# Performance work log

Measured on AMD Instinct MI355X. Metric: run time of the kernel, lower is better.

## Reference

```python
import jax, jax.numpy as jnp
import numpy as np

B, T, FEAT, H, E, NT, NH = 64, 256, 188, 512, 1024, 14, 8
HD = E // NH  # head dim = 128


def _gru_dir(x, w_ih, w_hh, b_ih, b_hh):
    # x: [T, B, in]; PyTorch GRU gate order: r, z, n
    xp = jnp.einsum('tbi,gi->tbg', x, w_ih) + b_ih  # [T,B,3H]

    def step(h, xt):
        hp = h @ w_hh.T + b_hh
        r = jax.nn.sigmoid(xt[..., :H] + hp[..., :H])
        z = jax.nn.sigmoid(xt[..., H:2 * H] + hp[..., H:2 * H])
        n = jnp.tanh(xt[..., 2 * H:] + r * hp[..., 2 * H:])
        h = (1 - z) * n + z * h
        return h, h

    h0 = jnp.zeros((x.shape[1], H), x.dtype)
    _, hs = jax.lax.scan(step, h0, xp)
    return hs  # [T,B,H]


def _bigru(x, wf, wb):
    f = _gru_dir(x, *wf)
    b = _gru_dir(x[::-1], *wb)[::-1]
    return jnp.concatenate([f, b], -1)  # [T,B,2H]


def _forward(features, ne_table, g1f, g1b, g2f, g2b, q_w, q_b, k_w, k_b, v_w, v_b,
             out_w, out_b, lin_w, lin_b, crf_start, crf_end, crf_trans, labels):
    nb = features.shape[0]
    x = features.transpose(1, 0, 2)  # [T,B,FEAT]
    enc = _bigru(x, g1f, g1b)        # [T,B,2H]=[T,B,E]
    # NE embedding: arange(14) rows for every batch element -> [S=14, B, 14]
    ne = jnp.broadcast_to(ne_table[:, None, :], (NT, nb, NT))
    # nn.MultiheadAttention with kdim=vdim=NT
    q = (enc @ q_w.T + q_b).reshape(T, nb, NH, HD)
    k = (ne @ k_w.T + k_b).reshape(NT, nb, NH, HD)
    v = (ne @ v_w.T + v_b).reshape(NT, nb, NH, HD)
    scores = jnp.einsum('tbhd,sbhd->bhts', q, k) / jnp.sqrt(jnp.float32(HD))
    attn = jax.nn.softmax(scores, axis=-1)
    ao = jnp.einsum('bhts,sbhd->tbhd', attn, v).reshape(T, nb, E)
    ao = ao @ out_w.T + out_b
    dec_in = jnp.concatenate([enc, ao], -1)   # [T,B,4H]
    dec = _bigru(dec_in, g2f, g2b)            # [T,B,2H]
    dec = dec @ lin_w.T + lin_b               # [T,B,NT]
    dec = dec.transpose(1, 0, 2)              # [B,T,NT]
    # scaled dot product against NE embeddings -> emissions [B,T,NT]
    logits = jnp.einsum('btd,sd->bts', dec, ne_table) / jnp.sqrt(jnp.float32(NT))
    # CRF negative log likelihood, reduction='mean', full mask
    em = jnp.take_along_axis(logits, labels[..., None], axis=2)[..., 0]  # [B,T]
    num = (crf_start[labels[:, 0]] + em.sum(1)
           + crf_trans[labels[:, :-1], labels[:, 1:]].sum(1)
           + crf_end[labels[:, -1]])
    alpha0 = crf_start + logits[:, 0]  # [B,NT]

    def step(a, e_t):
        a = jax.nn.logsumexp(a[:, :, None] + crf_trans[None] + e_t[:, None, :], axis=1)
        return a, None

    alpha, _ = jax.lax.scan(step, alpha0, logits[:, 1:].transpose(1, 0, 2))
    den = jax.nn.logsumexp(alpha + crf_end, axis=1)
    return -(num - den).mean()


def setup_inputs() -> dict:
    key = jax.random.key(0)
    ks = iter(jax.random.split(key, 40))

    def rn(shape, s=0.05):
        return jax.random.normal(next(ks), shape, jnp.float32) * s

    inp = {}
    inp['features'] = jax.random.normal(next(ks), (B, T, FEAT), jnp.float32)
    inp['labels'] = jax.random.randint(next(ks), (B, T), 0, NT)
    inp['ne_table'] = rn((NT, NT), 0.5).at[0].set(0.0)  # padding_idx=0
    for g, fi in (('gru1', FEAT), ('gru2', 4 * H)):
        for d in ('f', 'b'):
            inp[f'{g}_w_ih_{d}'] = rn((3 * H, fi))
            inp[f'{g}_w_hh_{d}'] = rn((3 * H, H))
            inp[f'{g}_b_ih_{d}'] = rn((3 * H,))
            inp[f'{g}_b_hh_{d}'] = rn((3 * H,))
    inp['q_w'] = rn((E, E)); inp['q_b'] = rn((E,))
    inp['k_w'] = rn((E, NT)); inp['k_b'] = rn((E,))
    inp['v_w'] = rn((E, NT)); inp['v_b'] = rn((E,))
    inp['out_w'] = rn((E, E)); inp['out_b'] = rn((E,))
    inp['lin_w'] = rn((NT, 2 * H)); inp['lin_b'] = rn((NT,))
    inp['crf_start'] = rn((NT,), 0.1)
    inp['crf_end'] = rn((NT,), 0.1)
    inp['crf_trans'] = rn((NT, NT), 0.1)
    return inp


def reference(features, labels, ne_table,
              gru1_w_ih_f, gru1_w_hh_f, gru1_b_ih_f, gru1_b_hh_f,
              gru1_w_ih_b, gru1_w_hh_b, gru1_b_ih_b, gru1_b_hh_b,
              gru2_w_ih_f, gru2_w_hh_f, gru2_b_ih_f, gru2_b_hh_f,
              gru2_w_ih_b, gru2_w_hh_b, gru2_b_ih_b, gru2_b_hh_b,
              q_w, q_b, k_w, k_b, v_w, v_b, out_w, out_b,
              lin_w, lin_b, crf_start, crf_end, crf_trans):
    return _forward(features, ne_table,
                    (gru1_w_ih_f, gru1_w_hh_f, gru1_b_ih_f, gru1_b_hh_f),
                    (gru1_w_ih_b, gru1_w_hh_b, gru1_b_ih_b, gru1_b_hh_b),
                    (gru2_w_ih_f, gru2_w_hh_f, gru2_b_ih_f, gru2_b_hh_f),
                    (gru2_w_ih_b, gru2_w_hh_b, gru2_b_ih_b, gru2_b_hh_b),
                    q_w, q_b, k_w, k_b, v_w, v_b, out_w, out_b,
                    lin_w, lin_b, crf_start, crf_end, crf_trans, labels)
```

## Files before the change

### kernel.cpp

```cpp
#include <hip/hip_runtime.h>
#include <hip/hip_bf16.h>
#include <math.h>

typedef __hip_bfloat16 bf16;
typedef __bf16 bf16x8 __attribute__((ext_vector_type(8)));
typedef float  f32x4  __attribute__((ext_vector_type(4)));
typedef unsigned long long u64;

#define T_SEQ 256
#define BATCH 64
#define FEATD 188
#define HID   512
#define EMB   1024
#define NTAG  14
#define G3    1536
#define GRU_NBLK 64
#define FLAG_LAYER (8 * T_SEQ * 32)

__global__ __launch_bounds__(256) void f32_to_bf16(
    const float* __restrict__ src, bf16* __restrict__ dst, int n4)
{
  int i = blockIdx.x * 256 + threadIdx.x;
  if (i >= n4) return;
  float4 v = *(const float4*)(src + (size_t)i * 4);
  bf16 o[4] = {__float2bfloat16(v.x), __float2bfloat16(v.y),
               __float2bfloat16(v.z), __float2bfloat16(v.w)};
  *(ushort4*)(dst + (size_t)i * 4) = *(ushort4*)o;
}

__global__ __launch_bounds__(256) void gemm_mfma(
    const bf16* __restrict__ A1, int lda1,
    const bf16* __restrict__ A2, int lda2, int K1,
    const bf16* __restrict__ W, int ldw,
    const float* __restrict__ bias,
    bf16* __restrict__ C, int ldc,
    int M, int N, int K)
{
  __shared__ __bf16 As[128][40];
  __shared__ __bf16 Bs[128][40];
  const int bm = blockIdx.y * 128;
  const int bn = blockIdx.x * 128;
  const int tid = threadIdx.x;
  const int wave = tid >> 6, lane = tid & 63;
  const int wr = wave >> 1, wc = wave & 1;
  const int lr = lane & 15, lk = (lane >> 4) << 3;
  f32x4 acc[4][4] = {};
  for (int k0 = 0; k0 < K; k0 += 32) {
#pragma unroll
    for (int p = 0; p < 4; ++p) {
      int i = tid + p * 256;
      int row = i >> 3, q = i & 7;
      int kg = k0 + q * 4;
      ushort4 va{0, 0, 0, 0}, vb{0, 0, 0, 0};
      if (kg < K) {
        const bf16* srca = (kg < K1) ? A1 + (size_t)(bm + row) * lda1 + kg
                                     : A2 + (size_t)(bm + row) * lda2 + (kg - K1);
        va = *(const ushort4*)srca;
        vb = *(const ushort4*)(W + (size_t)(bn + row) * ldw + kg);
      }
      *(ushort4*)&As[row][q * 4] = va;
      *(ushort4*)&Bs[row][q * 4] = vb;
    }
    __syncthreads();
    bf16x8 af[4], bf_[4];
#pragma unroll
    for (int i = 0; i < 4; ++i)
      af[i] = *(const bf16x8*)&As[wr * 64 + i * 16 + lr][lk];
#pragma unroll
    for (int j = 0; j < 4; ++j)
      bf_[j] = *(const bf16x8*)&Bs[wc * 64 + j * 16 + lr][lk];
#pragma unroll
    for (int i = 0; i < 4; ++i)
#pragma unroll
      for (int j = 0; j < 4; ++j)
        acc[i][j] = __builtin_amdgcn_mfma_f32_16x16x32_bf16(af[i], bf_[j], acc[i][j], 0, 0, 0);
    __syncthreads();
  }
#pragma unroll
  for (int j = 0; j < 4; ++j) {
    int n = bn + wc * 64 + j * 16 + lr;
    float bv = bias ? bias[n] : 0.f;
#pragma unroll
    for (int i = 0; i < 4; ++i) {
#pragma unroll
      for (int p = 0; p < 4; ++p) {
        int m = bm + wr * 64 + i * 16 + (lane >> 4) * 4 + p;
        C[(size_t)m * ldc + n] = __float2bfloat16(acc[i][j][p] + bv);
      }
    }
  }
}

__global__ __launch_bounds__(256) void transpose_feat(
    const float* __restrict__ f, bf16* __restrict__ xT)
{
  const int idx = blockIdx.x * 256 + threadIdx.x;
  const int total = BATCH * T_SEQ * FEATD;
  if (idx >= total) return;
  const int i = idx % FEATD;
  const int r = idx / FEATD;
  const int b = r / T_SEQ;
  const int t = r % T_SEQ;
  xT[((size_t)t * BATCH + b) * FEATD + i] = __float2bfloat16(f[idx]);
}

__global__ __launch_bounds__(256, 1) void gru_persist(
    const bf16* __restrict__ xp_f, const bf16* __restrict__ xp_b,
    const bf16* __restrict__ whh_f, const bf16* __restrict__ whh_b,
    const float* __restrict__ bhh_f, const float* __restrict__ bhh_b,
    bf16* __restrict__ out, int* __restrict__ flags)
{
  const int blk = blockIdx.x;
  const int dir = blk >> 5;
  const int ct  = blk & 31;
  const bf16* xp   = dir ? xp_b  : xp_f;
  const bf16* whh  = dir ? whh_b : whh_f;
  const float* bhh = dir ? bhh_b : bhh_f;
  const int off = dir ? HID : 0;
  const int tid = threadIdx.x;
  const int wave = tid >> 6, lane = tid & 63;
  const int lr = lane & 15, lkq = lane >> 4;
  int* fl = flags + (size_t)(dir * 4 + wave) * (T_SEQ * 32);

  __shared__ __bf16 Ws[48][520];
  for (int i = tid; i < 48 * 64; i += 256) {
    int r = i >> 6, q = i & 63;
    int grow = (r >> 4) * HID + ct * 16 + (r & 15);
    *(float4*)&Ws[r][q * 8] = *(const float4*)(whh + (size_t)grow * HID + q * 8);
  }
  __syncthreads();

  float bh[3];
#pragma unroll
  for (int g = 0; g < 3; ++g)
    bh[g] = bhh[g * HID + ct * 16 + lr];

  float hp[4] = {};

  bf16 xc[3][4];
  {
    const int t0 = dir ? (T_SEQ - 1) : 0;
    const size_t xb = (size_t)t0 * BATCH * G3;
#pragma unroll
    for (int p = 0; p < 4; ++p) {
      const size_t xrow = xb + (size_t)(wave * 16 + lkq * 4 + p) * G3;
#pragma unroll
      for (int g = 0; g < 3; ++g)
        xc[g][p] = xp[xrow + g * HID + ct * 16 + lr];
    }
  }

  for (int s = 0; s < T_SEQ; ++s) {
    const int t = dir ? (T_SEQ - 1 - s) : s;

    f32x4 acc[3] = {};
    if (s > 0) {
      int ready = 0;
      do {
        int f = 1;
        if (lane < 32)
          f = __hip_atomic_load(&fl[(s - 1) * 32 + lane],
                                __ATOMIC_RELAXED, __HIP_MEMORY_SCOPE_AGENT);
        ready = __all(f != 0);
        if (!ready) __builtin_amdgcn_s_sleep(1);
      } while (!ready);
      __builtin_amdgcn_sched_barrier(0);
      const int tp = dir ? t + 1 : t - 1;
      const bf16* arow = out + (size_t)tp * BATCH * EMB + off
                         + (size_t)(wave * 16 + lr) * EMB + lkq * 8;
      u64 h0[16], h1[16];
#pragma unroll
      for (int ki = 0; ki < 16; ++ki) {
        h0[ki] = __hip_atomic_load((const u64*)(arow + ki * 32),
                                   __ATOMIC_RELAXED, __HIP_MEMORY_SCOPE_AGENT);
        h1[ki] = __hip_atomic_load((const u64*)(arow + ki * 32 + 4),
                                   __ATOMIC_RELAXED, __HIP_MEMORY_SCOPE_AGENT);
      }
#pragma unroll
      for (int ki = 0; ki < 16; ++ki) {
        union { u64 v[2]; bf16x8 f; } ua;
        ua.v[0] = h0[ki]; ua.v[1] = h1[ki];
#pragma unroll
        for (int g = 0; g < 3; ++g) {
          bf16x8 b = *(const bf16x8*)&Ws[g * 16 + lr][ki * 32 + lkq * 8];
          acc[g] = __builtin_amdgcn_mfma_f32_16x16x32_bf16(ua.f, b, acc[g], 0, 0, 0);
        }
      }
    }

    const size_t obase = (size_t)t * BATCH * EMB + off;
    const int c = ct * 16 + lr;
#pragma unroll
    for (int p = 0; p < 4; ++p) {
      const int m = wave * 16 + lkq * 4 + p;
      float xr = __bfloat162float(xc[0][p]);
      float xz = __bfloat162float(xc[1][p]);
      float xn = __bfloat162float(xc[2][p]);
      float r = 1.f / (1.f + expf(-(xr + acc[0][p] + bh[0])));
      float z = 1.f / (1.f + expf(-(xz + acc[1][p] + bh[1])));
      float n = tanhf(xn + r * (acc[2][p] + bh[2]));
      float h = (1.f - z) * n + z * hp[p];
      hp[p] = h;
      bf16 hvb = __float2bfloat16(h);
      int mb = *(unsigned short*)&hvb;
      int pb = __shfl_xor(mb, 1);
      if (!(lr & 1)) {
        unsigned int pk = (unsigned int)mb | ((unsigned int)pb << 16);
        __hip_atomic_store((unsigned int*)(out + obase + (size_t)m * EMB + c), pk,
                           __ATOMIC_RELAXED, __HIP_MEMORY_SCOPE_AGENT);
      }
    }

    asm volatile("s_waitcnt vmcnt(0)" ::: "memory");
    if (s + 1 < T_SEQ) {
      if (lane == 0)
        __hip_atomic_store(&fl[s * 32 + ct], 1,
                           __ATOMIC_RELAXED, __HIP_MEMORY_SCOPE_AGENT);
      const int tn = dir ? (T_SEQ - 2 - s) : (s + 1);
      const size_t xb2 = (size_t)tn * BATCH * G3;
#pragma unroll
      for (int p = 0; p < 4; ++p) {
        const size_t xrow = xb2 + (size_t)(wave * 16 + lkq * 4 + p) * G3;
#pragma unroll
        for (int g = 0; g < 3; ++g)
          xc[g][p] = xp[xrow + g * HID + ct * 16 + lr];
      }
    }
  }
}

__global__ __launch_bounds__(256) void kv_kernel(
    const float* __restrict__ ne, const float* __restrict__ k_w,
    const float* __restrict__ k_b, const float* __restrict__ v_w,
    const float* __restrict__ v_b, float* __restrict__ kk,
    float* __restrict__ vv)
{
  const int e = blockIdx.x * 256 + threadIdx.x;
  if (e >= EMB) return;
#pragma unroll
  for (int s = 0; s < NTAG; ++s) {
    float a = k_b[e], c = v_b[e];
#pragma unroll
    for (int i = 0; i < NTAG; ++i) {
      float nv = ne[s * NTAG + i];
      a = fmaf(nv, k_w[e * NTAG + i], a);
      c = fmaf(nv, v_w[e * NTAG + i], c);
    }
    kk[s * EMB + e] = a;
    vv[s * EMB + e] = c;
  }
}

__global__ __launch_bounds__(256) void attn_kernel(
    const bf16* __restrict__ q, const float* __restrict__ kk,
    const float* __restrict__ vv, bf16* __restrict__ ao)
{
  const int unit = blockIdx.x * 4 + (threadIdx.x >> 6);
  const int h = unit & 7;
  const int tb = unit >> 3;
  const int lane = threadIdx.x & 63;
  const size_t qbase = (size_t)tb * EMB + h * 128;
  const int kbase = h * 128 + lane;
  float q0 = __bfloat162float(q[qbase + lane]);
  float q1 = __bfloat162float(q[qbase + 64 + lane]);
  float sc[NTAG];
#pragma unroll
  for (int j = 0; j < NTAG; ++j) {
    float p = q0 * kk[j * EMB + kbase] + q1 * kk[j * EMB + 64 + kbase];
#pragma unroll
    for (int d = 32; d; d >>= 1) p += __shfl_xor(p, d);
    sc[j] = p * 0.088388347648318447f;
  }
  float m = sc[0];
#pragma unroll
  for (int j = 1; j < NTAG; ++j) m = fmaxf(m, sc[j]);
  float sum = 0.f;
#pragma unroll
  for (int j = 0; j < NTAG; ++j) { sc[j] = expf(sc[j] - m); sum += sc[j]; }
  float inv = 1.f / sum;
  float o0 = 0.f, o1 = 0.f;
#pragma unroll
  for (int j = 0; j < NTAG; ++j) {
    float p = sc[j] * inv;
    o0 = fmaf(p, vv[j * EMB + kbase], o0);
    o1 = fmaf(p, vv[j * EMB + 64 + kbase], o1);
  }
  ao[qbase + lane] = __float2bfloat16(o0);
  ao[qbase + 64 + lane] = __float2bfloat16(o1);
}

__global__ __launch_bounds__(256) void dec_logits_kernel(
    const bf16* __restrict__ dec, const float* __restrict__ lin_w,
    const float* __restrict__ lin_b, const float* __restrict__ ne,
    float* __restrict__ logits)
{
  const int tb = blockIdx.x * 4 + (threadIdx.x >> 6);
  const int t = tb >> 6;
  const int b = tb & 63;
  const int lane = threadIdx.x & 63;
  const bf16* drow = dec + (size_t)tb * EMB;
  float dv[16];
#pragma unroll
  for (int i = 0; i < 16; ++i) dv[i] = __bfloat162float(drow[lane + 64 * i]);
  float dl[NTAG];
#pragma unroll
  for (int n = 0; n < NTAG; ++n) {
    float p = 0.f;
#pragma unroll
    for (int i = 0; i < 16; ++i)
      p = fmaf(dv[i], lin_w[n * EMB + lane + 64 * i], p);
#pragma unroll
    for (int d = 32; d; d >>= 1) p += __shfl_xor(p, d);
    dl[n] = p + lin_b[n];
  }
  if (lane < NTAG) {
    float acc = 0.f;
#pragma unroll
    for (int d2 = 0; d2 < NTAG; ++d2)
      acc = fmaf(dl[d2], ne[lane * NTAG + d2], acc);
    logits[((size_t)b * T_SEQ + t) * NTAG + lane] = acc * 0.26726124191242439f;
  }
}

__global__ __launch_bounds__(64) void crf_kernel(
    const float* __restrict__ logits, const int* __restrict__ labels,
    const float* __restrict__ cstart, const float* __restrict__ cend,
    const float* __restrict__ ctrans, float* __restrict__ lossb)
{
  const int b = blockIdx.x;
  const int lane = threadIdx.x;
  __shared__ float al[NTAG];
  __shared__ float tr[NTAG * NTAG];
  __shared__ float tmp[NTAG];
  const float* lg = logits + (size_t)b * T_SEQ * NTAG;
  const int* lab = labels + (size_t)b * T_SEQ;
  for (int i = lane; i < NTAG * NTAG; i += 64) tr[i] = ctrans[i];
  if (lane < NTAG) al[lane] = cstart[lane] + lg[lane];
  __syncthreads();
  for (int t = 1; t < T_SEQ; ++t) {
    float v = 0.f;
    if (lane < NTAG) {
      float mx = -1e30f;
#pragma unroll
      for (int i = 0; i < NTAG; ++i) mx = fmaxf(mx, al[i] + tr[i * NTAG + lane]);
      float sm = 0.f;
#pragma unroll
      for (int i = 0; i < NTAG; ++i) sm += expf(al[i] + tr[i * NTAG + lane] - mx);
      v = mx + logf(sm) + lg[t * NTAG + lane];
    }
    __syncthreads();
    if (lane < NTAG) al[lane] = v;
    __syncthreads();
  }
  float em = 0.f;
  for (int t = lane; t < T_SEQ; t += 64) em += lg[t * NTAG + lab[t]];
  float trs = 0.f;
  for (int t = lane; t < T_SEQ - 1; t += 64) trs += tr[lab[t] * NTAG + lab[t + 1]];
  float p = em + trs;
#pragma unroll
  for (int d = 32; d; d >>= 1) p += __shfl_xor(p, d);
  if (lane < NTAG) tmp[lane] = al[lane] + cend[lane];
  __syncthreads();
  if (lane == 0) {
    float num = p + cstart[lab[0]] + cend[lab[T_SEQ - 1]];
    float mx = tmp[0];
#pragma unroll
    for (int i = 1; i < NTAG; ++i) mx = fmaxf(mx, tmp[i]);
    float sm = 0.f;
#pragma unroll
    for (int i = 0; i < NTAG; ++i) sm += expf(tmp[i] - mx);
    float den = mx + logf(sm);
    lossb[b] = -(num - den);
  }
}

__global__ __launch_bounds__(64) void final_reduce(
    const float* __restrict__ lossb, float* __restrict__ out)
{
  float v = lossb[threadIdx.x];
#pragma unroll
  for (int d = 32; d; d >>= 1) v += __shfl_xor(v, d);
  if (threadIdx.x == 0) out[0] = v * (1.f / 64.f);
}

extern "C" void kernel_launch(void* const* d_in, const int* in_sizes, int n_in,
                              void* d_out, int out_size, void* d_ws, size_t ws_size,
                              hipStream_t stream)
{
  const float* features = (const float*)d_in[0];
  const int*   labels   = (const int*)d_in[1];
  const float* ne_table = (const float*)d_in[2];
  const float* g1_wih_f = (const float*)d_in[3];
  const float* g1_whh_f = (const float*)d_in[4];
  const float* g1_bih_f = (const float*)d_in[5];
  const float* g1_bhh_f = (const float*)d_in[6];
  const float* g1_wih_b = (const float*)d_in[7];
  const float* g1_whh_b = (const float*)d_in[8];
  const float* g1_bih_b = (const float*)d_in[9];
  const float* g1_bhh_b = (const float*)d_in[10];
  const float* g2_wih_f = (const float*)d_in[11];
  const float* g2_whh_f = (const float*)d_in[12];
  const float* g2_bih_f = (const float*)d_in[13];
  const float* g2_bhh_f = (const float*)d_in[14];
  const float* g2_wih_b = (const float*)d_in[15];
  const float* g2_whh_b = (const float*)d_in[16];
  const float* g2_bih_b = (const float*)d_in[17];
  const float* g2_bhh_b = (const float*)d_in[18];
  const float* q_w   = (const float*)d_in[19];
  const float* q_b   = (const float*)d_in[20];
  const float* k_w   = (const float*)d_in[21];
  const float* k_b   = (const float*)d_in[22];
  const float* v_w   = (const float*)d_in[23];
  const float* v_b   = (const float*)d_in[24];
  const float* out_w = (const float*)d_in[25];
  const float* out_b = (const float*)d_in[26];
  const float* lin_w = (const float*)d_in[27];
  const float* lin_b = (const float*)d_in[28];
  const float* crf_start = (const float*)d_in[29];
  const float* crf_end   = (const float*)d_in[30];
  const float* crf_trans = (const float*)d_in[31];

  const size_t NTB = (size_t)T_SEQ * BATCH;
  char* base = (char*)d_ws;
  size_t off = 0;
  auto alloc = [&](size_t bytes) {
    char* p = base + off;
    off += (bytes + 255) & ~(size_t)255;
    return p;
  };
  bf16* xpA  = (bf16*)alloc(NTB * G3 * sizeof(bf16));
  bf16* xpB  = (bf16*)alloc(NTB * G3 * sizeof(bf16));
  bf16* enc  = (bf16*)alloc(NTB * EMB * sizeof(bf16));
  bf16* bufD = (bf16*)alloc(NTB * EMB * sizeof(bf16));
  bf16* bufE = (bf16*)alloc(NTB * EMB * sizeof(bf16));
  float* kkbuf  = (float*)alloc((size_t)NTAG * EMB * sizeof(float));
  float* vvbuf  = (float*)alloc((size_t)NTAG * EMB * sizeof(float));
  float* logits = (float*)alloc(NTB * NTAG * sizeof(float));
  float* lossb  = (float*)alloc(64 * sizeof(float));
  int*   flags  = (int*)alloc(2 * FLAG_LAYER * sizeof(int));
  bf16* w1if = (bf16*)alloc((size_t)G3 * FEATD * sizeof(bf16));
  bf16* w1ib = (bf16*)alloc((size_t)G3 * FEATD * sizeof(bf16));
  bf16* w1hf = (bf16*)alloc((size_t)G3 * HID * sizeof(bf16));
  bf16* w1hb = (bf16*)alloc((size_t)G3 * HID * sizeof(bf16));
  bf16* w2if = (bf16*)alloc((size_t)G3 * 2 * EMB * sizeof(bf16));
  bf16* w2ib = (bf16*)alloc((size_t)G3 * 2 * EMB * sizeof(bf16));
  bf16* w2hf = (bf16*)alloc((size_t)G3 * HID * sizeof(bf16));
  bf16* w2hb = (bf16*)alloc((size_t)G3 * HID * sizeof(bf16));
  bf16* wq   = (bf16*)alloc((size_t)EMB * EMB * sizeof(bf16));
  bf16* wo   = (bf16*)alloc((size_t)EMB * EMB * sizeof(bf16));
  (void)off; (void)ws_size; (void)in_sizes; (void)n_in; (void)out_size;

  bf16* xT = bufD;

  const int M = (int)NTB;
  dim3 blk(256);

  hipMemsetAsync(flags, 0, 2 * FLAG_LAYER * sizeof(int), stream);

  auto conv = [&](const float* s, bf16* d, size_t n) {
    f32_to_bf16<<<(int)((n / 4 + 255) / 256), blk, 0, stream>>>(s, d, (int)(n / 4));
  };
  conv(g1_wih_f, w1if, (size_t)G3 * FEATD);
  conv(g1_wih_b, w1ib, (size_t)G3 * FEATD);
  conv(g1_whh_f, w1hf, (size_t)G3 * HID);
  conv(g1_whh_b, w1hb, (size_t)G3 * HID);
  conv(g2_wih_f, w2if, (size_t)G3 * 2 * EMB);
  conv(g2_wih_b, w2ib, (size_t)G3 * 2 * EMB);
  conv(g2_whh_f, w2hf, (size_t)G3 * HID);
  conv(g2_whh_b, w2hb, (size_t)G3 * HID);
  conv(q_w, wq, (size_t)EMB * EMB);
  conv(out_w, wo, (size_t)EMB * EMB);

  transpose_feat<<<(BATCH * T_SEQ * FEATD + 255) / 256, blk, 0, stream>>>(features, xT);

  dim3 g_xp(G3 / 128, M / 128);
  dim3 g_e(EMB / 128, M / 128);

  gemm_mfma<<<g_xp, blk, 0, stream>>>(xT, FEATD, nullptr, 0, FEATD,
                                      w1if, FEATD, g1_bih_f, xpA, G3, M, G3, FEATD);
  gemm_mfma<<<g_xp, blk, 0, stream>>>(xT, FEATD, nullptr, 0, FEATD,
                                      w1ib, FEATD, g1_bih_b, xpB, G3, M, G3, FEATD);

  gru_persist<<<GRU_NBLK, blk, 0, stream>>>(xpA, xpB, w1hf, w1hb,
                                            g1_bhh_f, g1_bhh_b, enc, flags);

  kv_kernel<<<4, blk, 0, stream>>>(ne_table, k_w, k_b, v_w, v_b, kkbuf, vvbuf);
  gemm_mfma<<<g_e, blk, 0, stream>>>(enc, EMB, nullptr, 0, EMB,
                                     wq, EMB, q_b, bufE, EMB, M, EMB, EMB);

  attn_kernel<<<M * 2, blk, 0, stream>>>(bufE, kkbuf, vvbuf, bufD);
  gemm_mfma<<<g_e, blk, 0, stream>>>(bufD, EMB, nullptr, 0, EMB,
                                     wo, EMB, out_b, bufE, EMB, M, EMB, EMB);

  gemm_mfma<<<g_xp, blk, 0, stream>>>(enc, EMB, bufE, EMB, EMB,
                                      w2if, 2 * EMB, g2_bih_f, xpA, G3, M, G3, 2 * EMB);
  gemm_mfma<<<g_xp, blk, 0, stream>>>(enc, EMB, bufE, EMB, EMB,
                                      w2ib, 2 * EMB, g2_bih_b, xpB, G3, M, G3, 2 * EMB);

  gru_persist<<<GRU_NBLK, blk, 0, stream>>>(xpA, xpB, w2hf, w2hb,
                                            g2_bhh_f, g2_bhh_b, bufD,
                                            flags + FLAG_LAYER);

  dec_logits_kernel<<<M / 4, blk, 0, stream>>>(bufD, lin_w, lin_b, ne_table, logits);

  crf_kernel<<<BATCH, 64, 0, stream>>>(logits, labels, crf_start, crf_end, crf_trans, lossb);
  final_reduce<<<1, 64, 0, stream>>>(lossb, (float*)d_out);
}
```

Before: 4.301 ms.

## Load GEMM tiles directly into LDS and pad feature dim to 192

The GEMM tile loads now use global_load_lds 16-byte direct-to-LDS transfers instead of staging through registers, and the LDS tiles become unpadded 32-wide rows. To keep every load aligned and in bounds, the input feature dimension is zero-padded from 188 to 192 in both the transposed features and the first-layer input weights, which also removes the K-bound check. The aim is to cut register traffic and instruction count in the GEMM loop. The cost is possible LDS bank conflicts from the unpadded layout, and the K-tail guard is gone, so every K must now be a multiple of 32.

```diff
diff --git a/kernel.cpp b/kernel.cpp
--- a/kernel.cpp
+++ b/kernel.cpp
@@ -6,10 +6,12 @@
 typedef __bf16 bf16x8 __attribute__((ext_vector_type(8)));
 typedef float  f32x4  __attribute__((ext_vector_type(4)));
 typedef unsigned long long u64;
+typedef unsigned int u32;
 
 #define T_SEQ 256
 #define BATCH 64
 #define FEATD 188
+#define FPAD  192
 #define HID   512
 #define EMB   1024
 #define NTAG  14
@@ -26,6 +28,17 @@
   bf16 o[4] = {__float2bfloat16(v.x), __float2bfloat16(v.y),
                __float2bfloat16(v.z), __float2bfloat16(v.w)};
   *(ushort4*)(dst + (size_t)i * 4) = *(ushort4*)o;
+}
+
+__global__ __launch_bounds__(256) void f32_to_bf16_pad(
+    const float* __restrict__ src, bf16* __restrict__ dst, int rows)
+{
+  int idx = blockIdx.x * 256 + threadIdx.x;
+  int total = rows * FPAD;
+  if (idx >= total) return;
+  int r = idx / FPAD, i = idx - r * FPAD;
+  float v = (i < FEATD) ? src[(size_t)r * FEATD + i] : 0.f;
+  dst[idx] = __float2bfloat16(v);
 }
 
 __global__ __launch_bounds__(256) void gemm_mfma(
@@ -36,39 +49,42 @@
     bf16* __restrict__ C, int ldc,
     int M, int N, int K)
 {
-  __shared__ __bf16 As[128][40];
-  __shared__ __bf16 Bs[128][40];
+  __shared__ __align__(16) __bf16 As[128 * 32];
+  __shared__ __align__(16) __bf16 Bs[128 * 32];
   const int bm = blockIdx.y * 128;
   const int bn = blockIdx.x * 128;
   const int tid = threadIdx.x;
   const int wave = tid >> 6, lane = tid & 63;
   const int wr = wave >> 1, wc = wave & 1;
   const int lr = lane & 15, lk = (lane >> 4) << 3;
+  const int srow = wave * 16 + (lane >> 2);
+  const int scol = (lane & 3) * 8;
   f32x4 acc[4][4] = {};
   for (int k0 = 0; k0 < K; k0 += 32) {
 #pragma unroll
-    for (int p = 0; p < 4; ++p) {
-      int i = tid + p * 256;
-      int row = i >> 3, q = i & 7;
-      int kg = k0 + q * 4;
-      ushort4 va{0, 0, 0, 0}, vb{0, 0, 0, 0};
-      if (kg < K) {
-        const bf16* srca = (kg < K1) ? A1 + (size_t)(bm + row) * lda1 + kg
-                                     : A2 + (size_t)(bm + row) * lda2 + (kg - K1);
-        va = *(const ushort4*)srca;
-        vb = *(const ushort4*)(W + (size_t)(bn + row) * ldw + kg);
-      }
-      *(ushort4*)&As[row][q * 4] = va;
-      *(ushort4*)&Bs[row][q * 4] = vb;
+    for (int j = 0; j < 2; ++j) {
+      const int row = srow + j * 64;
+      const int kg = k0 + scol;
+      const bf16* srca = (kg < K1) ? A1 + (size_t)(bm + row) * lda1 + kg
+                                   : A2 + (size_t)(bm + row) * lda2 + (kg - K1);
+      const bf16* srcb = W + (size_t)(bn + row) * ldw + kg;
+      __builtin_amdgcn_global_load_lds(
+          (const __attribute__((address_space(1))) u32*)srca,
+          (__attribute__((address_space(3))) u32*)(&As[j * 2048 + wave * 512]),
+          16, 0, 0);
+      __builtin_amdgcn_global_load_lds(
+          (const __attribute__((address_space(1))) u32*)srcb,
+          (__attribute__((address_space(3))) u32*)(&Bs[j * 2048 + wave * 512]),
+          16, 0, 0);
     }
     __syncthreads();
     bf16x8 af[4], bf_[4];
 #pragma unroll
     for (int i = 0; i < 4; ++i)
-      af[i] = *(const bf16x8*)&As[wr * 64 + i * 16 + lr][lk];
+      af[i] = *(const bf16x8*)&As[(wr * 64 + i * 16 + lr) * 32 + lk];
 #pragma unroll
     for (int j = 0; j < 4; ++j)
-      bf_[j] = *(const bf16x8*)&Bs[wc * 64 + j * 16 + lr][lk];
+      bf_[j] = *(const bf16x8*)&Bs[(wc * 64 + j * 16 + lr) * 32 + lk];
 #pragma unroll
     for (int i = 0; i < 4; ++i)
 #pragma unroll
@@ -95,13 +111,14 @@
     const float* __restrict__ f, bf16* __restrict__ xT)
 {
   const int idx = blockIdx.x * 256 + threadIdx.x;
-  const int total = BATCH * T_SEQ * FEATD;
+  const int total = BATCH * T_SEQ * FPAD;
   if (idx >= total) return;
-  const int i = idx % FEATD;
-  const int r = idx / FEATD;
-  const int b = r / T_SEQ;
-  const int t = r % T_SEQ;
-  xT[((size_t)t * BATCH + b) * FEATD + i] = __float2bfloat16(f[idx]);
+  const int i = idx % FPAD;
+  const int r = idx / FPAD;
+  const int t = r / BATCH;
+  const int b = r % BATCH;
+  float v = (i < FEATD) ? f[((size_t)b * T_SEQ + t) * FEATD + i] : 0.f;
+  xT[idx] = __float2bfloat16(v);
 }
 
 __global__ __launch_bounds__(256, 1) void gru_persist(
@@ -438,8 +455,8 @@
   float* logits = (float*)alloc(NTB * NTAG * sizeof(float));
   float* lossb  = (float*)alloc(64 * sizeof(float));
   int*   flags  = (int*)alloc(2 * FLAG_LAYER * sizeof(int));
-  bf16* w1if = (bf16*)alloc((size_t)G3 * FEATD * sizeof(bf16));
-  bf16* w1ib = (bf16*)alloc((size_t)G3 * FEATD * sizeof(bf16));
+  bf16* w1if = (bf16*)alloc((size_t)G3 * FPAD * sizeof(bf16));
+  bf16* w1ib = (bf16*)alloc((size_t)G3 * FPAD * sizeof(bf16));
   bf16* w1hf = (bf16*)alloc((size_t)G3 * HID * sizeof(bf16));
   bf16* w1hb = (bf16*)alloc((size_t)G3 * HID * sizeof(bf16));
   bf16* w2if = (bf16*)alloc((size_t)G3 * 2 * EMB * sizeof(bf16));
@@ -460,8 +477,8 @@
   auto conv = [&](const float* s, bf16* d, size_t n) {
     f32_to_bf16<<<(int)((n / 4 + 255) / 256), blk, 0, stream>>>(s, d, (int)(n / 4));
   };
-  conv(g1_wih_f, w1if, (size_t)G3 * FEATD);
-  conv(g1_wih_b, w1ib, (size_t)G3 * FEATD);
+  f32_to_bf16_pad<<<(G3 * FPAD + 255) / 256, blk, 0, stream>>>(g1_wih_f, w1if, G3);
+  f32_to_bf16_pad<<<(G3 * FPAD + 255) / 256, blk, 0, stream>>>(g1_wih_b, w1ib, G3);
   conv(g1_whh_f, w1hf, (size_t)G3 * HID);
   conv(g1_whh_b, w1hb, (size_t)G3 * HID);
   conv(g2_wih_f, w2if, (size_t)G3 * 2 * EMB);
@@ -471,15 +488,15 @@
   conv(q_w, wq, (size_t)EMB * EMB);
   conv(out_w, wo, (size_t)EMB * EMB);
 
-  transpose_feat<<<(BATCH * T_SEQ * FEATD + 255) / 256, blk, 0, stream>>>(features, xT);
+  transpose_feat<<<(BATCH * T_SEQ * FPAD + 255) / 256, blk, 0, stream>>>(features, xT);
 
   dim3 g_xp(G3 / 128, M / 128);
   dim3 g_e(EMB / 128, M / 128);
 
-  gemm_mfma<<<g_xp, blk, 0, stream>>>(xT, FEATD, nullptr, 0, FEATD,
-                                      w1if, FEATD, g1_bih_f, xpA, G3, M, G3, FEATD);
-  gemm_mfma<<<g_xp, blk, 0, stream>>>(xT, FEATD, nullptr, 0, FEATD,
-                                      w1ib, FEATD, g1_bih_b, xpB, G3, M, G3, FEATD);
+  gemm_mfma<<<g_xp, blk, 0, stream>>>(xT, FPAD, nullptr, 0, FPAD,
+                                      w1if, FPAD, g1_bih_f, xpA, G3, M, G3, FPAD);
+  gemm_mfma<<<g_xp, blk, 0, stream>>>(xT, FPAD, nullptr, 0, FPAD,
+                                      w1ib, FPAD, g1_bih_b, xpB, G3, M, G3, FPAD);
 
   gru_persist<<<GRU_NBLK, blk, 0, stream>>>(xpA, xpB, w1hf, w1hb,
                                             g1_bhh_f, g1_bhh_b, enc, flags);
```

Measured after the change: 4.151 ms. 1.04x faster.
